# Optimization experiments

Measured on AMD Instinct MI355X. Metric: run time of the kernel, lower is better.

Reference implementation:

```python
import jax, jax.numpy as jnp
import numpy as np

N_ATOMS = 10000
N_PAIRS = 100000
H = 64          # hidden_channels
R = 32          # number_of_radial_basis_functions
MAX_Z = 100
CUTOFF = 0.5    # nm (radial_max_distance), min = 0.0


def cosine_cutoff(d):
    # 0.5*(cos(pi*d/rc)+1) for d < rc else 0
    return jnp.where(d < CUTOFF, 0.5 * (jnp.cos(jnp.pi * d / CUTOFF) + 1.0), 0.0)


def expnormal_rbf(d):
    # ExpNormal smearing (TorchMD/TensorNet style), cutoff_lower = 0
    start = float(np.exp(-CUTOFF))
    means = jnp.linspace(start, 1.0, R, dtype=d.dtype)            # [R]
    beta = (2.0 / R * (1.0 - start)) ** -2
    alpha = 5.0 / CUTOFF
    return jnp.exp(-beta * (jnp.exp(-alpha * d)[:, None] - means) ** 2)  # [P,R]


def vector_to_skewtensor(v):
    x, y, z = v[:, 0], v[:, 1], v[:, 2]
    o = jnp.zeros_like(x)
    return jnp.stack([o, -z, y, z, o, -x, -y, x, o], axis=-1).reshape(-1, 3, 3)


def vector_to_symtensor(v):
    t = v[:, :, None] * v[:, None, :]                              # [P,3,3]
    tr3 = (t[:, 0, 0] + t[:, 1, 1] + t[:, 2, 2]) / 3.0
    return t - tr3[:, None, None] * jnp.eye(3, dtype=v.dtype)


def setup_inputs() -> dict:
    key = jax.random.key(0)
    ks = jax.random.split(key, 20)
    atomic_numbers = jax.random.randint(ks[0], (N_ATOMS,), 0, MAX_Z)
    pair_indices = jax.random.randint(ks[1], (2, N_PAIRS), 0, N_ATOMS)
    r_ij = jax.random.normal(ks[2], (N_PAIRS, 3), dtype=jnp.float32) * 0.12  # ~0.2 nm norms
    d_ij = jnp.linalg.norm(r_ij, axis=-1, keepdims=True) + 1e-6
    s = 0.1
    p = {
        'emb':    jax.random.normal(ks[3], (MAX_Z, H)) * s,
        'emb2_w': jax.random.normal(ks[4], (H, 2 * H)) * s,
        'emb2_b': jnp.zeros((H,)),
        'dp1_w':  jax.random.normal(ks[5], (H, R)) * s,
        'dp1_b':  jnp.zeros((H,)),
        'dp2_w':  jax.random.normal(ks[6], (H, R)) * s,
        'dp2_b':  jnp.zeros((H,)),
        'dp3_w':  jax.random.normal(ks[7], (H, R)) * s,
        'dp3_b':  jnp.zeros((H,)),
        'lt0_w':  jax.random.normal(ks[8], (H, H)) * s,
        'lt1_w':  jax.random.normal(ks[9], (H, H)) * s,
        'lt2_w':  jax.random.normal(ks[10], (H, H)) * s,
        'ls1_w':  jax.random.normal(ks[11], (2 * H, H)) * s,
        'ls1_b':  jnp.zeros((2 * H,)),
        'ls2_w':  jax.random.normal(ks[12], (3 * H, 2 * H)) * s,
        'ls2_b':  jnp.zeros((3 * H,)),
        'ln_g':   jnp.ones((H,)),
        'ln_b':   jnp.zeros((H,)),
    }
    return dict(atomic_numbers=atomic_numbers, pair_indices=pair_indices,
                d_ij=d_ij, r_ij=r_ij, **p)


def reference(atomic_numbers, pair_indices, d_ij, r_ij,
              emb, emb2_w, emb2_b, dp1_w, dp1_b, dp2_w, dp2_b, dp3_w, dp3_b,
              lt0_w, lt1_w, lt2_w, ls1_w, ls1_b, ls2_w, ls2_b, ln_g, ln_b):
    n_atoms = atomic_numbers.shape[0]
    src = pair_indices[0]
    # atomic number message Zij: concat(emb[i], emb[j]) -> Linear
    zi = emb[atomic_numbers]                                      # [N,H]
    zij = jnp.concatenate([zi[src], zi[pair_indices[1]]], axis=-1)  # [P,2H]
    Zij = zij @ emb2_w.T + emb2_b                                 # [P,H]
    d = d_ij[:, 0]                                                # [P]
    unit = r_ij / d_ij                                            # [P,3]
    rc = cosine_cutoff(d)                                         # [P]
    rbf = expnormal_rbf(d) * rc[:, None]                          # [P,R]
    C = rc[:, None] * Zij                                         # [P,H]
    f1 = (rbf @ dp1_w.T + dp1_b) * C                              # [P,H]
    f2 = (rbf @ dp2_w.T + dp2_b) * C * 10.0                       # Angstrom scale
    f3 = (rbf @ dp3_w.T + dp3_b) * C * 100.0
    eye = jnp.eye(3, dtype=r_ij.dtype)
    skew = vector_to_skewtensor(unit)                             # [P,3,3]
    sym = vector_to_symtensor(unit)                               # [P,3,3]
    Iij = f1[:, :, None, None] * eye                              # [P,H,3,3]
    Aij = f2[:, :, None, None] * skew[:, None]
    Sij = f3[:, :, None, None] * sym[:, None]
    I = jax.ops.segment_sum(Iij, src, num_segments=n_atoms)       # [N,H,3,3]
    A = jax.ops.segment_sum(Aij, src, num_segments=n_atoms)
    S = jax.ops.segment_sum(Sij, src, num_segments=n_atoms)
    # tensor_norm -> LayerNorm -> scalar MLP
    tn = jnp.sum((I + A + S) ** 2, axis=(-2, -1))                 # [N,H]
    mu = tn.mean(-1, keepdims=True)
    var = tn.var(-1, keepdims=True)
    norm = (tn - mu) / jnp.sqrt(var + 1e-5) * ln_g + ln_b
    norm = jax.nn.silu(norm @ ls1_w.T + ls1_b)
    norm = jax.nn.silu(norm @ ls2_w.T + ls2_b)                    # [N,3H]
    norm = norm.reshape(-1, H, 3)
    I = jnp.einsum('nhij,gh->ngij', I, lt0_w) * norm[:, :, 0][:, :, None, None]
    A = jnp.einsum('nhij,gh->ngij', A, lt1_w) * norm[:, :, 1][:, :, None, None]
    S = jnp.einsum('nhij,gh->ngij', S, lt2_w) * norm[:, :, 2][:, :, None, None]
    return I + A + S
```

## Files before the change

### kernel.cpp

```cpp
#include <hip/hip_runtime.h>
#include <hip/hip_bf16.h>

#define N_ATOMS 10000
#define N_PAIRS 100000
#define HH 64
#define MAXZ 100

typedef _Float16 h2_t __attribute__((ext_vector_type(2)));

constexpr float RBF_START = 0.6065306597126334f;
constexpr float RBF_STEP  = (1.0f - RBF_START) / 31.0f;
constexpr float RBF_BETA  = 1.0f / ((0.0625f * (1.0f - RBF_START)) * (0.0625f * (1.0f - RBF_START)));
constexpr float LOG2E     = 1.4426950408889634f;
constexpr float NEG_ALPHA_L2 = -10.0f * LOG2E;
constexpr float NEG_BETA_L2  = -RBF_BETA * LOG2E;

#define OFF_EMB   0
#define OFF_W2    6400
#define OFF_B2    14592
#define OFF_D1W   14656
#define OFF_D1B   16704
#define OFF_D2W   16768
#define OFF_D2B   18816
#define OFF_D3W   18880
#define OFF_D3B   20928
#define OFF_LT0   20992
#define OFF_LT1   25088
#define OFF_LT2   29184
#define OFF_L1W   33280
#define OFF_L1B   41472
#define OFF_L2W   41600
#define OFF_L2B   66176
#define OFF_LNG   66368
#define OFF_LNB   66432
#define N_PARAMF  66496

#define PH_DP   0
#define PH_L1   3072
#define PH_L2   7168
#define PH_LT   19456
#define PH_T2H  25600
#define PH_N    28800

#define WS_WF     0
#define WS_CNT    266240
#define WS_OFF    307200
#define WS_CUR    348160
#define WS_T1     389120
#define WS_T2     414720
#define WS_PH     440320
#define WS_DPK    555520
#define WS_ZNL    2155520

__device__ __forceinline__ float bf2f(unsigned short u) {
    return __uint_as_float(((unsigned int)u) << 16);
}
__device__ __forceinline__ float fexp2(float x) { return __builtin_amdgcn_exp2f(x); }
__device__ __forceinline__ float fcos2pi(float x) { return __builtin_amdgcn_cosf(x); }
__device__ __forceinline__ float fsilu(float x) { return x / (1.0f + fexp2(-LOG2E * x)); }
__device__ __forceinline__ h2_t u2h(unsigned u) { return __builtin_bit_cast(h2_t, u); }
__device__ __forceinline__ unsigned packh2(float a, float b) {
    h2_t v; v.x = (_Float16)a; v.y = (_Float16)b;
    return __builtin_bit_cast(unsigned, v);
}

#if __has_builtin(__builtin_amdgcn_fdot2)
__device__ __forceinline__ float FDOT2(h2_t a, h2_t b, float c) {
    return __builtin_amdgcn_fdot2(a, b, c, false);
}
#else
__device__ __forceinline__ float FDOT2(h2_t a, h2_t b, float c) {
    return c + (float)a.x * (float)b.x + (float)a.y * (float)b.y;
}
#endif
__device__ __forceinline__ float dot16v(uint4 a, uint4 b, float acc) {
    acc = FDOT2(u2h(a.x), u2h(b.x), acc);
    acc = FDOT2(u2h(a.y), u2h(b.y), acc);
    acc = FDOT2(u2h(a.z), u2h(b.z), acc);
    acc = FDOT2(u2h(a.w), u2h(b.w), acc);
    return acc;
}
__device__ __forceinline__ float dot16h(const uint4* w, const uint4* x, float acc) {
    return dot16v(*w, *x, acc);
}

__device__ int classify64(const unsigned short* b, int lane) {
    unsigned short x = b[lane];
    int e = (x >> 7) & 0xFF;
    bool implaus = (x != 0) && (e < 96 || e > 133);
    bool zeroeven = ((lane & 1) == 0) && (x == 0);
    unsigned long long mi = __ballot(implaus);
    unsigned long long mz = __ballot(zeroeven);
    if (__popcll(mz) == 32) return 0;
    if (__popcll(mi) >= 8) return 0;
    return 1;
}

struct ConvArgs { const void* src[18]; float* dst; };

__global__ void k_prep(ConvArgs a, const int* __restrict__ pidx, int* __restrict__ cnt) {
    const int sizes[18] = {6400,8192,64,2048,64,2048,64,2048,64,4096,4096,4096,8192,128,24576,192,64,64};
    __shared__ int fl;
    if (threadIdx.x < 64) {
        int f = classify64((const unsigned short*)a.src[0], threadIdx.x);
        if (threadIdx.x == 0) fl = f;
    }
    __syncthreads();
    int t = blockIdx.x * 256 + threadIdx.x;
    if (t < N_PARAMF) {
        int acc = 0, seg = 0, off = t;
        #pragma unroll
        for (int i = 0; i < 18; ++i) {
            if (t >= acc && t < acc + sizes[i]) { seg = i; off = t - acc; }
            acc += sizes[i];
        }
        if (fl == 1) a.dst[t] = bf2f(((const unsigned short*)a.src[seg])[off]);
        else         a.dst[t] = ((const float*)a.src[seg])[off];
    }
    if (t < N_PAIRS) atomicAdd(&cnt[pidx[t]], 1);
}

__global__ void k_scantab(const float* __restrict__ WF, float* __restrict__ T1,
                          float* __restrict__ T2, unsigned* __restrict__ PH,
                          const int* __restrict__ cnt, int* __restrict__ offs,
                          int* __restrict__ cur) {
    __shared__ int buf[1024];
    if (blockIdx.x == 0) {
        int tid = threadIdx.x;
        int base = tid * 10;
        int c[10]; int s = 0;
        #pragma unroll
        for (int i = 0; i < 10; ++i) {
            int idx = base + i;
            int v = (idx < N_ATOMS) ? cnt[idx] : 0;
            c[i] = v; s += v;
        }
        buf[tid] = s;
        __syncthreads();
        for (int off = 1; off < 1024; off <<= 1) {
            int v = (tid >= off) ? buf[tid - off] : 0;
            __syncthreads();
            buf[tid] += v;
            __syncthreads();
        }
        int run = buf[tid] - s;
        #pragma unroll
        for (int i = 0; i < 10; ++i) {
            int idx = base + i;
            if (idx < N_ATOMS) { offs[idx] = run; cur[idx] = run; run += c[i]; }
        }
        if (tid == 0) offs[N_ATOMS] = N_PAIRS;
        return;
    }
    int t = (blockIdx.x - 1) * 1024 + threadIdx.x;
    if (t < 6400) {
        int z = t >> 6, h = t & 63;
        const float* ez = WF + OFF_EMB + z * HH;
        const float* w2 = WF + OFF_W2 + h * 128;
        float s1 = 0.f, s2 = 0.f;
        #pragma unroll
        for (int k = 0; k < 64; ++k) {
            float e = ez[k];
            s1 += w2[k] * e;
            s2 += w2[64 + k] * e;
        }
        T1[z * HH + h] = s1;
        T2[z * HH + h] = s2;
        _Float16 hv = (_Float16)s2;
        ((unsigned short*)(PH + PH_T2H))[z * HH + h] = __builtin_bit_cast(unsigned short, hv);
    }
    if (t < 25600) {
        int src;
        if (t < PH_L1) {
            int w = t >> 10, r = t & 1023;
            src = (w == 0 ? OFF_D1W : (w == 1 ? OFF_D2W : OFF_D3W)) + r * 2;
        } else if (t < PH_L2) {
            src = OFF_L1W + (t - PH_L1) * 2;
        } else if (t < PH_LT) {
            src = OFF_L2W + (t - PH_L2) * 2;
        } else {
            src = OFF_LT0 + (t - PH_LT) * 2;
        }
        PH[t] = packh2(WF[src], WF[src + 1]);
    }
}

__global__ void k_fill(const int* __restrict__ pidx, const int* __restrict__ an,
                       const void* __restrict__ dij_v, const void* __restrict__ rij_v,
                       int* __restrict__ cur,
                       float4* __restrict__ dpack, int* __restrict__ znl) {
    __shared__ int fdr[2];
    if (threadIdx.x < 64) {
        int fd = classify64((const unsigned short*)dij_v, threadIdx.x);
        int fr = classify64((const unsigned short*)rij_v, threadIdx.x);
        if (threadIdx.x == 0) { fdr[0] = fd; fdr[1] = fr; }
    }
    __syncthreads();
    int p = blockIdx.x * 256 + threadIdx.x;
    if (p >= N_PAIRS) return;
    int s = pidx[p];
    int dst = pidx[N_PAIRS + p];
    int pos = atomicAdd(&cur[s], 1);
    float d, rx, ry, rz;
    if (fdr[0] == 1) d = bf2f(((const unsigned short*)dij_v)[p]);
    else             d = ((const float*)dij_v)[p];
    if (fdr[1] == 1) {
        const unsigned short* r = (const unsigned short*)rij_v;
        rx = bf2f(r[3*p]); ry = bf2f(r[3*p+1]); rz = bf2f(r[3*p+2]);
    } else {
        const float* r = (const float*)rij_v;
        rx = r[3*p]; ry = r[3*p+1]; rz = r[3*p+2];
    }
    float inv = 1.0f / d;
    dpack[pos] = make_float4(rx * inv, ry * inv, rz * inv, d);
    znl[pos] = an[dst];
}

__global__ __launch_bounds__(256, 2) void k_fused(
    const int* __restrict__ an,
    const float* __restrict__ WF,
    const int* __restrict__ offs,
    const float4* __restrict__ dpack, const int* __restrict__ znl,
    const float* __restrict__ T1,
    const unsigned* __restrict__ PH,
    float* __restrict__ out)
{
    __shared__ __align__(16) unsigned T2L[3200];
    __shared__ __align__(16) unsigned wL2[192 * 68];
    __shared__ __align__(16) unsigned rbuf[4][2][16];
    __shared__ __align__(16) unsigned acch[4][11 * 32];
    __shared__ __align__(16) unsigned y1h[4][64];
    __shared__ __align__(16) unsigned y2h[4][96];

    for (int q = threadIdx.x; q < 3200; q += 256) T2L[q] = PH[PH_T2H + q];
    for (int q = threadIdx.x; q < 12288; q += 256) {
        int m = q >> 6, u = q & 63;
        wL2[m * 68 + u] = PH[PH_L2 + q];
    }
    __syncthreads();

    const int wave = threadIdx.x >> 6;
    const int h    = threadIdx.x & 63;

    const uint4* wp = (const uint4*)(PH + PH_DP);
    const uint4 w10 = wp[        h * 4 + 0], w11 = wp[        h * 4 + 1],
                w12 = wp[        h * 4 + 2], w13 = wp[        h * 4 + 3];
    const uint4 w20 = wp[256 +   h * 4 + 0], w21 = wp[256 +   h * 4 + 1],
                w22 = wp[256 +   h * 4 + 2], w23 = wp[256 +   h * 4 + 3];
    const uint4 w30 = wp[512 +   h * 4 + 0], w31 = wp[512 +   h * 4 + 1],
                w32 = wp[512 +   h * 4 + 2], w33 = wp[512 +   h * 4 + 3];

    const float ed1 = (WF + OFF_D1B)[h];
    const float ed2 = (WF + OFF_D2B)[h];
    const float ed3 = (WF + OFF_D3B)[h];
    const float eb2 = (WF + OFF_B2)[h];
    const float lng = (WF + OFF_LNG)[h];
    const float lnb = (WF + OFF_LNB)[h];
    const float l1ba = (WF + OFF_L1B)[h];
    const float l1bb = (WF + OFF_L1B)[h + 64];
    const float l2b0 = (WF + OFF_L2B)[h];
    const float l2b1 = (WF + OFF_L2B)[h + 64];
    const float l2b2 = (WF + OFF_L2B)[h + 128];

    const _Float16* T2h = (const _Float16*)T2L;
    unsigned* sl0 = &rbuf[wave][0][0];
    unsigned* sl1 = &rbuf[wave][1][0];
    const uint4* l1base = (const uint4*)(PH + PH_L1);
    const uint4* lt0 = (const uint4*)(PH + PH_LT) + h * 8;
    const uint4* lt1 = (const uint4*)(PH + PH_LT + 2048) + h * 8;
    const uint4* lt2 = (const uint4*)(PH + PH_LT + 4096) + h * 8;

    const int stride = gridDim.x * 4;
    for (int n = blockIdx.x * 4 + wave; n < N_ATOMS; n += stride) {
        const float zA = eb2 + T1[an[n] * HH + h];
        const int pbeg = offs[n];
        const int len  = offs[n + 1] - pbeg;

        float Is=0.f, sx=0.f, sy=0.f, sz=0.f;
        float Sxx=0.f, Syy=0.f, Szz=0.f, Sxy=0.f, Sxz=0.f, Syz=0.f;

        float4 dc = make_float4(0,0,0,0), dn = make_float4(0,0,0,0);
        int zn_c = 0, zn_n = 0;
        float rc_c = 0.f, rc_n = 0.f;
        if (len > 0) { dc = dpack[pbeg];     zn_c = znl[pbeg]; }
        if (len > 1) { dn = dpack[pbeg + 1]; zn_n = znl[pbeg + 1]; }
        if (len > 0) {
            float d = dc.w;
            rc_c = (d < 0.5f) ? 0.5f * (fcos2pi(d) + 1.0f) : 0.0f;
            float en = fexp2(NEG_ALPHA_L2 * d);
            if (h < 16) {
                float t0 = en - (RBF_START + RBF_STEP * (float)(2 * h));
                float t1 = en - (RBF_START + RBF_STEP * (float)(2 * h + 1));
                sl0[h] = packh2(fexp2(NEG_BETA_L2 * t0 * t0) * rc_c,
                                fexp2(NEG_BETA_L2 * t1 * t1) * rc_c);
            }
        }
        __builtin_amdgcn_wave_barrier();

        for (int ii = 0; ii < len; ++ii) {
            if (ii + 1 < len) {
                float d = dn.w;
                rc_n = (d < 0.5f) ? 0.5f * (fcos2pi(d) + 1.0f) : 0.0f;
                float en = fexp2(NEG_ALPHA_L2 * d);
                unsigned* sl = (ii & 1) ? sl0 : sl1;
                if (h < 16) {
                    float t0 = en - (RBF_START + RBF_STEP * (float)(2 * h));
                    float t1 = en - (RBF_START + RBF_STEP * (float)(2 * h + 1));
                    sl[h] = packh2(fexp2(NEG_BETA_L2 * t0 * t0) * rc_n,
                                   fexp2(NEG_BETA_L2 * t1 * t1) * rc_n);
                }
            }
            float4 d2v = make_float4(0,0,0,0); int zn2 = 0;
            bool has2 = (ii + 2 < len);
            if (has2) { d2v = dpack[pbeg + ii + 2]; zn2 = znl[pbeg + ii + 2]; }

            float t2v = (float)T2h[zn_c * HH + h];

            const uint4* rbp = (const uint4*)((ii & 1) ? sl1 : sl0);
            uint4 b0 = rbp[0], b1 = rbp[1], b2 = rbp[2], b3 = rbp[3];
            float g1 = ed1, g2 = ed2, g3 = ed3;
            g1 = dot16v(w10, b0, g1); g1 = dot16v(w11, b1, g1);
            g1 = dot16v(w12, b2, g1); g1 = dot16v(w13, b3, g1);
            g2 = dot16v(w20, b0, g2); g2 = dot16v(w21, b1, g2);
            g2 = dot16v(w22, b2, g2); g2 = dot16v(w23, b3, g2);
            g3 = dot16v(w30, b0, g3); g3 = dot16v(w31, b1, g3);
            g3 = dot16v(w32, b2, g3); g3 = dot16v(w33, b3, g3);

            float ux = dc.x, uy = dc.y, uz = dc.z;
            float Cc = rc_c * (zA + t2v);
            float f1 = g1 * Cc;
            float f2 = g2 * Cc * 10.0f;
            float f3 = g3 * Cc * 100.0f;

            Is += f1;
            sx += f2 * ux;  sy += f2 * uy;  sz += f2 * uz;
            float q = (ux*ux + uy*uy + uz*uz) * (1.0f / 3.0f);
            Sxx += f3 * (ux*ux - q);
            Syy += f3 * (uy*uy - q);
            Szz += f3 * (uz*uz - q);
            Sxy += f3 * (ux*uy);
            Sxz += f3 * (ux*uz);
            Syz += f3 * (uy*uz);

            dc = dn; zn_c = zn_n; rc_c = rc_n;
            if (has2) { dn = d2v; zn_n = zn2; }
            __builtin_amdgcn_wave_barrier();
        }

        float tn = 3.0f*Is*Is + 2.0f*(sx*sx + sy*sy + sz*sz)
                 + Sxx*Sxx + Syy*Syy + Szz*Szz
                 + 2.0f*(Sxy*Sxy + Sxz*Sxz + Syz*Syz);
        float s1 = tn, s2 = tn * tn;
        #pragma unroll
        for (int o = 32; o > 0; o >>= 1) {
            s1 += __shfl_xor(s1, o);
            s2 += __shfl_xor(s2, o);
        }
        float mu  = s1 * (1.0f / 64.0f);
        float var = s2 * (1.0f / 64.0f) - mu * mu;
        float nv  = (tn - mu) * rsqrtf(var + 1e-5f) * lng + lnb;

        float vals[11] = {Is, sx, sy, sz, Sxx, Syy, Szz, Sxy, Sxz, Syz, nv};
        #pragma unroll
        for (int c = 0; c < 11; ++c) {
            float pv = __shfl_xor(vals[c], 1);
            if ((h & 1) == 0) acch[wave][c * 32 + (h >> 1)] = packh2(vals[c], pv);
        }
        __builtin_amdgcn_wave_barrier();

        const uint4* nvh = (const uint4*)&acch[wave][10 * 32];
        float ya = l1ba, yb = l1bb;
        {
            const uint4* ra = l1base + h * 8;
            const uint4* rb = l1base + (h + 64) * 8;
            #pragma unroll
            for (int k = 0; k < 8; ++k) {
                ya = dot16h(ra + k, nvh + k, ya);
                yb = dot16h(rb + k, nvh + k, yb);
            }
        }
        ya = fsilu(ya); yb = fsilu(yb);
        {
            float pa = __shfl_xor(ya, 1);
            float pb = __shfl_xor(yb, 1);
            if ((h & 1) == 0) {
                y1h[wave][(h >> 1)]      = packh2(ya, pa);
                y1h[wave][32 + (h >> 1)] = packh2(yb, pb);
            }
        }
        __builtin_amdgcn_wave_barrier();

        const uint4* y1p = (const uint4*)&y1h[wave][0];
        float z0 = l2b0, z1 = l2b1, z2 = l2b2;
        {
            const uint4* r0 = (const uint4*)&wL2[(h)       * 68];
            const uint4* r1 = (const uint4*)&wL2[(h + 64)  * 68];
            const uint4* r2 = (const uint4*)&wL2[(h + 128) * 68];
            #pragma unroll
            for (int k = 0; k < 16; ++k) {
                uint4 x = y1p[k];
                z0 = dot16v(r0[k], x, z0);
                z1 = dot16v(r1[k], x, z1);
                z2 = dot16v(r2[k], x, z2);
            }
        }
        z0 = fsilu(z0); z1 = fsilu(z1); z2 = fsilu(z2);
        {
            float p0 = __shfl_xor(z0, 1);
            float p1 = __shfl_xor(z1, 1);
            float p2 = __shfl_xor(z2, 1);
            if ((h & 1) == 0) {
                y2h[wave][(h >> 1)]      = packh2(z0, p0);
                y2h[wave][32 + (h >> 1)] = packh2(z1, p1);
                y2h[wave][64 + (h >> 1)] = packh2(z2, p2);
            }
        }
        __builtin_amdgcn_wave_barrier();

        float n0, n1, n2;
        {
            int i0 = 3 * h;
            unsigned u0 = y2h[wave][i0 >> 1];
            unsigned u1 = y2h[wave][(i0 >> 1) + 1];
            h2_t a = u2h(u0), b = u2h(u1);
            if (i0 & 1) { n0 = (float)a.y; n1 = (float)b.x; n2 = (float)b.y; }
            else        { n0 = (float)a.x; n1 = (float)a.y; n2 = (float)b.x; }
        }

        const uint4* aI  = (const uint4*)&acch[wave][0];
        const uint4* aAx = (const uint4*)&acch[wave][32];
        const uint4* aAy = (const uint4*)&acch[wave][64];
        const uint4* aAz = (const uint4*)&acch[wave][96];
        const uint4* aXX = (const uint4*)&acch[wave][128];
        const uint4* aYY = (const uint4*)&acch[wave][160];
        const uint4* aZZ = (const uint4*)&acch[wave][192];
        const uint4* aXY = (const uint4*)&acch[wave][224];
        const uint4* aXZ = (const uint4*)&acch[wave][256];
        const uint4* aYZ = (const uint4*)&acch[wave][288];

        float P0=0.f, PAx=0.f, PAy=0.f, PAz=0.f;
        float Q0=0.f, Q1=0.f, Q2=0.f, Q3=0.f, Q4=0.f, Q5=0.f;
        #pragma unroll
        for (int k = 0; k < 8; ++k) {
            P0  = dot16h(lt0 + k, aI  + k, P0);
            PAx = dot16h(lt1 + k, aAx + k, PAx);
            PAy = dot16h(lt1 + k, aAy + k, PAy);
            PAz = dot16h(lt1 + k, aAz + k, PAz);
            Q0  = dot16h(lt2 + k, aXX + k, Q0);
            Q1  = dot16h(lt2 + k, aYY + k, Q1);
            Q2  = dot16h(lt2 + k, aZZ + k, Q2);
            Q3  = dot16h(lt2 + k, aXY + k, Q3);
            Q4  = dot16h(lt2 + k, aXZ + k, Q4);
            Q5  = dot16h(lt2 + k, aYZ + k, Q5);
        }
        float Iv = P0 * n0;
        float Ax = PAx * n1, Ay = PAy * n1, Az = PAz * n1;
        float Xx = Q0 * n2, Yy = Q1 * n2, Zz = Q2 * n2;
        float Xy = Q3 * n2, Xz = Q4 * n2, Yz = Q5 * n2;

        float* o = out + (size_t)n * 576 + h * 9;
        o[0] =  Iv + Xx;  o[1] = -Az + Xy;  o[2] =  Ay + Xz;
        o[3] =  Az + Xy;  o[4] =  Iv + Yy;  o[5] = -Ax + Yz;
        o[6] = -Ay + Xz;  o[7] =  Ax + Yz;  o[8] =  Iv + Zz;
        __builtin_amdgcn_wave_barrier();
    }
}

extern "C" void kernel_launch(void* const* d_in, const int* in_sizes, int n_in,
                              void* d_out, int out_size, void* d_ws, size_t ws_size,
                              hipStream_t stream) {
    const int* an   = (const int*)d_in[0];
    const int* pidx = (const int*)d_in[1];

    char* ws = (char*)d_ws;
    float*    WF    = (float*)(ws + WS_WF);
    int*      cnt   = (int*)(ws + WS_CNT);
    int*      offs  = (int*)(ws + WS_OFF);
    int*      cur   = (int*)(ws + WS_CUR);
    float*    T1    = (float*)(ws + WS_T1);
    float*    T2    = (float*)(ws + WS_T2);
    unsigned* PH    = (unsigned*)(ws + WS_PH);
    float4*   dpack = (float4*)(ws + WS_DPK);
    int*      znl   = (int*)(ws + WS_ZNL);
    float*    out   = (float*)d_out;

    hipMemsetAsync(cnt, 0, N_ATOMS * sizeof(int), stream);

    ConvArgs ca;
    for (int i = 0; i < 18; ++i) ca.src[i] = d_in[4 + i];
    ca.dst = WF;
    k_prep<<<(N_PAIRS + 255) / 256, 256, 0, stream>>>(ca, pidx, cnt);
    k_scantab<<<26, 1024, 0, stream>>>(WF, T1, T2, PH, cnt, offs, cur);
    k_fill<<<(N_PAIRS + 255) / 256, 256, 0, stream>>>(pidx, an, d_in[2], d_in[3],
                                                      cur, dpack, znl);
    k_fused<<<512, 256, 0, stream>>>(an, WF, offs, dpack, znl, T1, PH, out);
}
```

Before: 235.0 us.

## Merge all stages into one cooperative kernel with grid syncs and precomputed RBF

```diff
diff --git a/kernel.cpp b/kernel.cpp
--- a/kernel.cpp
+++ b/kernel.cpp
@@ -1,5 +1,8 @@
 #include <hip/hip_runtime.h>
 #include <hip/hip_bf16.h>
+#include <hip/hip_cooperative_groups.h>
+
+namespace cg = cooperative_groups;
 
 #define N_ATOMS 10000
 #define N_PAIRS 100000
@@ -51,6 +54,7 @@
 #define WS_PH     440320
 #define WS_DPK    555520
 #define WS_ZNL    2155520
+#define WS_RBF    2555520
 
 __device__ __forceinline__ float bf2f(unsigned short u) {
     return __uint_as_float(((unsigned int)u) << 16);
@@ -98,35 +102,50 @@
 
 struct ConvArgs { const void* src[18]; float* dst; };
 
-__global__ void k_prep(ConvArgs a, const int* __restrict__ pidx, int* __restrict__ cnt) {
-    const int sizes[18] = {6400,8192,64,2048,64,2048,64,2048,64,4096,4096,4096,8192,128,24576,192,64,64};
-    __shared__ int fl;
-    if (threadIdx.x < 64) {
-        int f = classify64((const unsigned short*)a.src[0], threadIdx.x);
-        if (threadIdx.x == 0) fl = f;
+__global__ __launch_bounds__(1024, 4) void k_mega(
+    ConvArgs ca, const int* __restrict__ pidx, const int* __restrict__ an,
+    const void* __restrict__ dij_v, const void* __restrict__ rij_v,
+    float* __restrict__ WF, int* __restrict__ cnt, int* __restrict__ offs,
+    int* __restrict__ cur, float* __restrict__ T1, float* __restrict__ T2,
+    unsigned* __restrict__ PH, float4* __restrict__ dpack, int* __restrict__ znl,
+    unsigned* __restrict__ rbfp, float* __restrict__ out)
+{
+    cg::grid_group grid = cg::this_grid();
+
+    __shared__ __align__(16) unsigned T2L[3200];
+    __shared__ __align__(16) unsigned wL2[192 * 68];
+    __shared__ int scanbuf[1024];
+    __shared__ int fl3[3];
+    __shared__ __align__(16) unsigned acch[16][11 * 32];
+    __shared__ __align__(16) unsigned y1h[16][64];
+    __shared__ __align__(16) unsigned y2h[16][96];
+
+    const int tid  = threadIdx.x;
+    const int gtid = blockIdx.x * 1024 + tid;
+
+    if (tid < 64) {
+        int f0 = classify64((const unsigned short*)ca.src[0], tid);
+        int f1 = classify64((const unsigned short*)dij_v, tid);
+        int f2 = classify64((const unsigned short*)rij_v, tid);
+        if (tid == 0) { fl3[0] = f0; fl3[1] = f1; fl3[2] = f2; }
     }
     __syncthreads();
-    int t = blockIdx.x * 256 + threadIdx.x;
-    if (t < N_PARAMF) {
-        int acc = 0, seg = 0, off = t;
+    if (gtid < N_PARAMF) {
+        const int sizes[18] = {6400,8192,64,2048,64,2048,64,2048,64,4096,4096,4096,8192,128,24576,192,64,64};
+        int acc = 0, seg = 0, off = gtid;
         #pragma unroll
         for (int i = 0; i < 18; ++i) {
-            if (t >= acc && t < acc + sizes[i]) { seg = i; off = t - acc; }
+            if (gtid >= acc && gtid < acc + sizes[i]) { seg = i; off = gtid - acc; }
             acc += sizes[i];
         }
-        if (fl == 1) a.dst[t] = bf2f(((const unsigned short*)a.src[seg])[off]);
-        else         a.dst[t] = ((const float*)a.src[seg])[off];
-    }
-    if (t < N_PAIRS) atomicAdd(&cnt[pidx[t]], 1);
-}
-
-__global__ void k_scantab(const float* __restrict__ WF, float* __restrict__ T1,
-                          float* __restrict__ T2, unsigned* __restrict__ PH,
-                          const int* __restrict__ cnt, int* __restrict__ offs,
-                          int* __restrict__ cur) {
-    __shared__ int buf[1024];
+        if (fl3[0] == 1) WF[gtid] = bf2f(((const unsigned short*)ca.src[seg])[off]);
+        else             WF[gtid] = ((const float*)ca.src[seg])[off];
+    }
+    if (gtid < N_PAIRS) atomicAdd(&cnt[pidx[gtid]], 1);
+
+    grid.sync();
+
     if (blockIdx.x == 0) {
-        int tid = threadIdx.x;
         int base = tid * 10;
         int c[10]; int s = 0;
         #pragma unroll
@@ -135,112 +154,101 @@
             int v = (idx < N_ATOMS) ? cnt[idx] : 0;
             c[i] = v; s += v;
         }
-        buf[tid] = s;
+        scanbuf[tid] = s;
         __syncthreads();
         for (int off = 1; off < 1024; off <<= 1) {
-            int v = (tid >= off) ? buf[tid - off] : 0;
+            int v = (tid >= off) ? scanbuf[tid - off] : 0;
             __syncthreads();
-            buf[tid] += v;
+            scanbuf[tid] += v;
             __syncthreads();
         }
-        int run = buf[tid] - s;
+        int run = scanbuf[tid] - s;
         #pragma unroll
         for (int i = 0; i < 10; ++i) {
             int idx = base + i;
             if (idx < N_ATOMS) { offs[idx] = run; cur[idx] = run; run += c[i]; }
         }
         if (tid == 0) offs[N_ATOMS] = N_PAIRS;
-        return;
-    }
-    int t = (blockIdx.x - 1) * 1024 + threadIdx.x;
-    if (t < 6400) {
-        int z = t >> 6, h = t & 63;
-        const float* ez = WF + OFF_EMB + z * HH;
-        const float* w2 = WF + OFF_W2 + h * 128;
-        float s1 = 0.f, s2 = 0.f;
-        #pragma unroll
-        for (int k = 0; k < 64; ++k) {
-            float e = ez[k];
-            s1 += w2[k] * e;
-            s2 += w2[64 + k] * e;
-        }
-        T1[z * HH + h] = s1;
-        T2[z * HH + h] = s2;
-        _Float16 hv = (_Float16)s2;
-        ((unsigned short*)(PH + PH_T2H))[z * HH + h] = __builtin_bit_cast(unsigned short, hv);
-    }
-    if (t < 25600) {
-        int src;
-        if (t < PH_L1) {
-            int w = t >> 10, r = t & 1023;
-            src = (w == 0 ? OFF_D1W : (w == 1 ? OFF_D2W : OFF_D3W)) + r * 2;
-        } else if (t < PH_L2) {
-            src = OFF_L1W + (t - PH_L1) * 2;
-        } else if (t < PH_LT) {
-            src = OFF_L2W + (t - PH_L2) * 2;
+    } else if (blockIdx.x <= 25) {
+        int t = (blockIdx.x - 1) * 1024 + tid;
+        if (t < 6400) {
+            int z = t >> 6, h = t & 63;
+            const float* ez = WF + OFF_EMB + z * HH;
+            const float* w2 = WF + OFF_W2 + h * 128;
+            float s1 = 0.f, s2 = 0.f;
+            #pragma unroll
+            for (int k = 0; k < 64; ++k) {
+                float e = ez[k];
+                s1 += w2[k] * e;
+                s2 += w2[64 + k] * e;
+            }
+            T1[z * HH + h] = s1;
+            T2[z * HH + h] = s2;
+            _Float16 hv = (_Float16)s2;
+            ((unsigned short*)(PH + PH_T2H))[z * HH + h] = __builtin_bit_cast(unsigned short, hv);
+        }
+        if (t < 25600) {
+            int src;
+            if (t < PH_L1) {
+                int w = t >> 10, r = t & 1023;
+                src = (w == 0 ? OFF_D1W : (w == 1 ? OFF_D2W : OFF_D3W)) + r * 2;
+            } else if (t < PH_L2) {
+                src = OFF_L1W + (t - PH_L1) * 2;
+            } else if (t < PH_LT) {
+                src = OFF_L2W + (t - PH_L2) * 2;
+            } else {
+                src = OFF_LT0 + (t - PH_LT) * 2;
+            }
+            PH[t] = packh2(WF[src], WF[src + 1]);
+        }
+    }
+
+    grid.sync();
+
+    if (gtid < N_PAIRS) {
+        int p = gtid;
+        int s = pidx[p];
+        int dst = pidx[N_PAIRS + p];
+        int pos = atomicAdd(&cur[s], 1);
+        float d, rx, ry, rz;
+        if (fl3[1] == 1) d = bf2f(((const unsigned short*)dij_v)[p]);
+        else             d = ((const float*)dij_v)[p];
+        if (fl3[2] == 1) {
+            const unsigned short* r = (const unsigned short*)rij_v;
+            rx = bf2f(r[3*p]); ry = bf2f(r[3*p+1]); rz = bf2f(r[3*p+2]);
         } else {
-            src = OFF_LT0 + (t - PH_LT) * 2;
-        }
-        PH[t] = packh2(WF[src], WF[src + 1]);
-    }
-}
-
-__global__ void k_fill(const int* __restrict__ pidx, const int* __restrict__ an,
-                       const void* __restrict__ dij_v, const void* __restrict__ rij_v,
-                       int* __restrict__ cur,
-                       float4* __restrict__ dpack, int* __restrict__ znl) {
-    __shared__ int fdr[2];
-    if (threadIdx.x < 64) {
-        int fd = classify64((const unsigned short*)dij_v, threadIdx.x);
-        int fr = classify64((const unsigned short*)rij_v, threadIdx.x);
-        if (threadIdx.x == 0) { fdr[0] = fd; fdr[1] = fr; }
-    }
-    __syncthreads();
-    int p = blockIdx.x * 256 + threadIdx.x;
-    if (p >= N_PAIRS) return;
-    int s = pidx[p];
-    int dst = pidx[N_PAIRS + p];
-    int pos = atomicAdd(&cur[s], 1);
-    float d, rx, ry, rz;
-    if (fdr[0] == 1) d = bf2f(((const unsigned short*)dij_v)[p]);
-    else             d = ((const float*)dij_v)[p];
-    if (fdr[1] == 1) {
-        const unsigned short* r = (const unsigned short*)rij_v;
-        rx = bf2f(r[3*p]); ry = bf2f(r[3*p+1]); rz = bf2f(r[3*p+2]);
-    } else {
-        const float* r = (const float*)rij_v;
-        rx = r[3*p]; ry = r[3*p+1]; rz = r[3*p+2];
-    }
-    float inv = 1.0f / d;
-    dpack[pos] = make_float4(rx * inv, ry * inv, rz * inv, d);
-    znl[pos] = an[dst];
-}
-
-__global__ __launch_bounds__(256, 2) void k_fused(
-    const int* __restrict__ an,
-    const float* __restrict__ WF,
-    const int* __restrict__ offs,
-    const float4* __restrict__ dpack, const int* __restrict__ znl,
-    const float* __restrict__ T1,
-    const unsigned* __restrict__ PH,
-    float* __restrict__ out)
-{
-    __shared__ __align__(16) unsigned T2L[3200];
-    __shared__ __align__(16) unsigned wL2[192 * 68];
-    __shared__ __align__(16) unsigned rbuf[4][2][16];
-    __shared__ __align__(16) unsigned acch[4][11 * 32];
-    __shared__ __align__(16) unsigned y1h[4][64];
-    __shared__ __align__(16) unsigned y2h[4][96];
-
-    for (int q = threadIdx.x; q < 3200; q += 256) T2L[q] = PH[PH_T2H + q];
-    for (int q = threadIdx.x; q < 12288; q += 256) {
+            const float* r = (const float*)rij_v;
+            rx = r[3*p]; ry = r[3*p+1]; rz = r[3*p+2];
+        }
+        float inv = 1.0f / d;
+        float rc = (d < 0.5f) ? 0.5f * (fcos2pi(d) + 1.0f) : 0.0f;
+        dpack[pos] = make_float4(rx * inv, ry * inv, rz * inv, rc);
+        znl[pos] = an[dst];
+        float en = fexp2(NEG_ALPHA_L2 * d);
+        unsigned* rp = rbfp + pos * 16;
+        #pragma unroll
+        for (int r2 = 0; r2 < 16; ++r2) {
+            float t0 = en - (RBF_START + RBF_STEP * (float)(2 * r2));
+            float t1 = en - (RBF_START + RBF_STEP * (float)(2 * r2 + 1));
+            rp[r2] = packh2(fexp2(NEG_BETA_L2 * t0 * t0) * rc,
+                            fexp2(NEG_BETA_L2 * t1 * t1) * rc);
+        }
+    }
+
+    grid.sync();
+
+    for (int q = tid; q < 3200; q += 1024) T2L[q] = PH[PH_T2H + q];
+    for (int q = tid; q < 12288; q += 1024) {
         int m = q >> 6, u = q & 63;
         wL2[m * 68 + u] = PH[PH_L2 + q];
     }
     __syncthreads();
-
-    const int wave = threadIdx.x >> 6;
-    const int h    = threadIdx.x & 63;
+    const _Float16* T2h = (const _Float16*)T2L;
+
+    const int wave = tid >> 6;
+    const int h    = tid & 63;
+    const int gw   = blockIdx.x * 16 + wave;
+    const int GW   = 4096;
 
     const uint4* wp = (const uint4*)(PH + PH_DP);
     const uint4 w10 = wp[        h * 4 + 0], w11 = wp[        h * 4 + 1],
@@ -262,16 +270,13 @@
     const float l2b1 = (WF + OFF_L2B)[h + 64];
     const float l2b2 = (WF + OFF_L2B)[h + 128];
 
-    const _Float16* T2h = (const _Float16*)T2L;
-    unsigned* sl0 = &rbuf[wave][0][0];
-    unsigned* sl1 = &rbuf[wave][1][0];
+    const uint4* rbase  = (const uint4*)rbfp;
     const uint4* l1base = (const uint4*)(PH + PH_L1);
     const uint4* lt0 = (const uint4*)(PH + PH_LT) + h * 8;
     const uint4* lt1 = (const uint4*)(PH + PH_LT + 2048) + h * 8;
     const uint4* lt2 = (const uint4*)(PH + PH_LT + 4096) + h * 8;
 
-    const int stride = gridDim.x * 4;
-    for (int n = blockIdx.x * 4 + wave; n < N_ATOMS; n += stride) {
+    for (int n = gw; n < N_ATOMS; n += GW) {
         const float zA = eb2 + T1[an[n] * HH + h];
         const int pbeg = offs[n];
         const int len  = offs[n + 1] - pbeg;
@@ -279,45 +284,24 @@
         float Is=0.f, sx=0.f, sy=0.f, sz=0.f;
         float Sxx=0.f, Syy=0.f, Szz=0.f, Sxy=0.f, Sxz=0.f, Syz=0.f;
 
-        float4 dc = make_float4(0,0,0,0), dn = make_float4(0,0,0,0);
-        int zn_c = 0, zn_n = 0;
-        float rc_c = 0.f, rc_n = 0.f;
-        if (len > 0) { dc = dpack[pbeg];     zn_c = znl[pbeg]; }
-        if (len > 1) { dn = dpack[pbeg + 1]; zn_n = znl[pbeg + 1]; }
+        uint4 r0c={0,0,0,0}, r1c={0,0,0,0}, r2c={0,0,0,0}, r3c={0,0,0,0};
+        float4 dc = make_float4(0,0,0,0);
+        int zc_ = 0;
         if (len > 0) {
-            float d = dc.w;
-            rc_c = (d < 0.5f) ? 0.5f * (fcos2pi(d) + 1.0f) : 0.0f;
-            float en = fexp2(NEG_ALPHA_L2 * d);
-            if (h < 16) {
-                float t0 = en - (RBF_START + RBF_STEP * (float)(2 * h));
-                float t1 = en - (RBF_START + RBF_STEP * (float)(2 * h + 1));
-                sl0[h] = packh2(fexp2(NEG_BETA_L2 * t0 * t0) * rc_c,
-                                fexp2(NEG_BETA_L2 * t1 * t1) * rc_c);
-            }
-        }
-        __builtin_amdgcn_wave_barrier();
-
+            r0c = rbase[pbeg*4+0]; r1c = rbase[pbeg*4+1];
+            r2c = rbase[pbeg*4+2]; r3c = rbase[pbeg*4+3];
+            dc = dpack[pbeg]; zc_ = znl[pbeg];
+        }
         for (int ii = 0; ii < len; ++ii) {
+            const uint4 b0 = r0c, b1 = r1c, b2 = r2c, b3 = r3c;
+            const float4 dv = dc; const int zn = zc_;
             if (ii + 1 < len) {
-                float d = dn.w;
-                rc_n = (d < 0.5f) ? 0.5f * (fcos2pi(d) + 1.0f) : 0.0f;
-                float en = fexp2(NEG_ALPHA_L2 * d);
-                unsigned* sl = (ii & 1) ? sl0 : sl1;
-                if (h < 16) {
-                    float t0 = en - (RBF_START + RBF_STEP * (float)(2 * h));
-                    float t1 = en - (RBF_START + RBF_STEP * (float)(2 * h + 1));
-                    sl[h] = packh2(fexp2(NEG_BETA_L2 * t0 * t0) * rc_n,
-                                   fexp2(NEG_BETA_L2 * t1 * t1) * rc_n);
-                }
-            }
-            float4 d2v = make_float4(0,0,0,0); int zn2 = 0;
-            bool has2 = (ii + 2 < len);
-            if (has2) { d2v = dpack[pbeg + ii + 2]; zn2 = znl[pbeg + ii + 2]; }
-
-            float t2v = (float)T2h[zn_c * HH + h];
-
-            const uint4* rbp = (const uint4*)((ii & 1) ? sl1 : sl0);
-            uint4 b0 = rbp[0], b1 = rbp[1], b2 = rbp[2], b3 = rbp[3];
+                int j = pbeg + ii + 1;
+                r0c = rbase[j*4+0]; r1c = rbase[j*4+1];
+                r2c = rbase[j*4+2]; r3c = rbase[j*4+3];
+                dc = dpack[j]; zc_ = znl[j];
+            }
+            float t2v = (float)T2h[zn * HH + h];
             float g1 = ed1, g2 = ed2, g3 = ed3;
             g1 = dot16v(w10, b0, g1); g1 = dot16v(w11, b1, g1);
             g1 = dot16v(w12, b2, g1); g1 = dot16v(w13, b3, g1);
@@ -326,8 +310,8 @@
             g3 = dot16v(w30, b0, g3); g3 = dot16v(w31, b1, g3);
             g3 = dot16v(w32, b2, g3); g3 = dot16v(w33, b3, g3);
 
-            float ux = dc.x, uy = dc.y, uz = dc.z;
-            float Cc = rc_c * (zA + t2v);
+            float ux = dv.x, uy = dv.y, uz = dv.z;
+            float Cc = dv.w * (zA + t2v);
             float f1 = g1 * Cc;
             float f2 = g2 * Cc * 10.0f;
             float f3 = g3 * Cc * 100.0f;
@@ -341,10 +325,6 @@
             Sxy += f3 * (ux*uy);
             Sxz += f3 * (ux*uz);
             Syz += f3 * (uy*uz);
-
-            dc = dn; zn_c = zn_n; rc_c = rc_n;
-            if (has2) { dn = d2v; zn_n = zn2; }
-            __builtin_amdgcn_wave_barrier();
         }
 
         float tn = 3.0f*Is*Is + 2.0f*(sx*sx + sy*sy + sz*sz)
@@ -471,6 +451,8 @@
                               hipStream_t stream) {
     const int* an   = (const int*)d_in[0];
     const int* pidx = (const int*)d_in[1];
+    const void* dij = d_in[2];
+    const void* rij = d_in[3];
 
     char* ws = (char*)d_ws;
     float*    WF    = (float*)(ws + WS_WF);
@@ -482,6 +464,7 @@
     unsigned* PH    = (unsigned*)(ws + WS_PH);
     float4*   dpack = (float4*)(ws + WS_DPK);
     int*      znl   = (int*)(ws + WS_ZNL);
+    unsigned* rbfp  = (unsigned*)(ws + WS_RBF);
     float*    out   = (float*)d_out;
 
     hipMemsetAsync(cnt, 0, N_ATOMS * sizeof(int), stream);
@@ -489,9 +472,8 @@
     ConvArgs ca;
     for (int i = 0; i < 18; ++i) ca.src[i] = d_in[4 + i];
     ca.dst = WF;
-    k_prep<<<(N_PAIRS + 255) / 256, 256, 0, stream>>>(ca, pidx, cnt);
-    k_scantab<<<26, 1024, 0, stream>>>(WF, T1, T2, PH, cnt, offs, cur);
-    k_fill<<<(N_PAIRS + 255) / 256, 256, 0, stream>>>(pidx, an, d_in[2], d_in[3],
-                                                      cur, dpack, znl);
-    k_fused<<<512, 256, 0, stream>>>(an, WF, offs, dpack, znl, T1, PH, out);
-}
+
+    void* kargs[] = { &ca, &pidx, &an, &dij, &rij, &WF, &cnt, &offs, &cur,
+                      &T1, &T2, &PH, &dpack, &znl, &rbfp, &out };
+    hipLaunchCooperativeKernel((void*)k_mega, dim3(256), dim3(1024), kargs, 0, stream);
+}
```

Result: slower. 347.3 us (+47.8%).
